# Performance work log

Measured on AMD Instinct MI355X. Metric: run time of the kernel, lower is better.

## Reference

```python
import jax, jax.numpy as jnp
import numpy as np

GRID_W, GRID_H = 4, 4          # num_splits = (4, 4) -> 16 experts
N = 524288                     # number of sample points
IN_DIM, HID, OUT = 2, 256, 3   # per-expert MLP: 2 -> 256 -> 3


def setup_inputs() -> dict:
    key = jax.random.key(0)
    k_s, k_w1, k_w2 = jax.random.split(key, 3)
    E = GRID_W * GRID_H
    samples = jax.random.uniform(k_s, (N, IN_DIM), dtype=jnp.float32)
    W1 = jax.random.normal(k_w1, (E, IN_DIM, HID), dtype=jnp.float32) * (1.0 / np.sqrt(IN_DIM))
    b1 = jnp.zeros((E, HID), dtype=jnp.float32)
    W2 = jax.random.normal(k_w2, (E, HID, OUT), dtype=jnp.float32) * (1.0 / np.sqrt(HID))
    b2 = jnp.zeros((E, OUT), dtype=jnp.float32)
    return {"samples": samples, "W1": W1, "b1": b1, "W2": W2, "b2": b2}


def _grid_inds(samples):
    # i, j = floor(samples[:, d] * n).clip(0, n-1); inds = j * w + i
    i = jnp.clip(jnp.floor(samples[:, 0] * GRID_W), 0, GRID_W - 1)
    j = jnp.clip(jnp.floor(samples[:, 1] * GRID_H), 0, GRID_H - 1)
    return (j * GRID_W + i).astype(jnp.int32)  # [N]


def reference(samples, W1, b1, W2, b2):
    inds = _grid_inds(samples)                     # [N] expert id per sample
    E = W1.shape[0]
    out = jnp.zeros((samples.shape[0], W2.shape[-1]), dtype=samples.dtype)
    # Dense dispatch: loop over the small fixed set of experts (16) and
    # select each sample's own expert output via the routing mask. Same
    # math as torch's features[inds == i] gather + scatter combine.
    for e in range(E):
        h = jax.nn.relu(samples @ W1[e] + b1[e])   # [N, HID]
        y = h @ W2[e] + b2[e]                      # [N, OUT]
        out = jnp.where((inds == e)[:, None], y, out)
    return out
```

## Files before the change

### kernel.cpp

```cpp
#include <hip/hip_runtime.h>

typedef _Float16 h2 __attribute__((ext_vector_type(2)));

#define GRID_W 4
#define GRID_H 4
#define NEXP   16
#define HID    256
#define TPB    1024
#define S      2
#define SAMP   (TPB * S)
#define NWAVE  (TPB / 64)
#define WPE    1536
#define GR     192
#define MAXENT 32

#define NSLOT   (SAMP + GR)
#define OFFB_Y  (NSLOT * 8)
#define OFFB_I  (OFFB_Y + SAMP * 12)
#define LDS_BYTES (OFFB_I + 4 * (16 + 17 + 17 + 3 * MAXENT + 1))

__global__ __launch_bounds__(256) void convert_kernel(
    const float* __restrict__ W1, const float* __restrict__ b1,
    const float* __restrict__ W2, _Float16* __restrict__ wsW) {
    int t = blockIdx.x * 256 + threadIdx.x;
    int e = t >> 8, k = t & 255;
    _Float16* dst = wsW + e * WPE;
    dst[k]        = (_Float16)W1[e * 512 + k];
    dst[256 + k]  = (_Float16)W1[e * 512 + 256 + k];
    dst[512 + k]  = (_Float16)b1[e * 256 + k];
    dst[768 + k]  = (_Float16)W2[e * 768 + 3 * k];
    dst[1024 + k] = (_Float16)W2[e * 768 + 3 * k + 1];
    dst[1280 + k] = (_Float16)W2[e * 768 + 3 * k + 2];
}

union H8 { float4 f; h2 p[4]; };

template<int M>
__device__ __forceinline__ void mlp_pass(const float4* __restrict__ W4,
                                         const h2* px2, const h2* py2,
                                         float (*y)[3]) {
#pragma unroll 4
    for (int b = 0; b < 32; ++b) {
        H8 wa, wb, bb, u0, u1, u2;
        wa.f = W4[b];
        wb.f = W4[32 + b];
        bb.f = W4[64 + b];
        u0.f = W4[96 + b];
        u1.f = W4[128 + b];
        u2.f = W4[160 + b];
#pragma unroll
        for (int j = 0; j < 4; ++j) {
#pragma unroll
            for (int s = 0; s < M; ++s) {
                h2 h = __builtin_elementwise_fma(px2[s], wa.p[j],
                       __builtin_elementwise_fma(py2[s], wb.p[j], bb.p[j]));
                h2 z = (h2)(_Float16)0.0f;
                h = __builtin_elementwise_max(h, z);
                y[s][0] = __builtin_amdgcn_fdot2(h, u0.p[j], y[s][0], false);
                y[s][1] = __builtin_amdgcn_fdot2(h, u1.p[j], y[s][1], false);
                y[s][2] = __builtin_amdgcn_fdot2(h, u2.p[j], y[s][2], false);
            }
        }
    }
}

__global__ __launch_bounds__(TPB) void fused_moe_kernel(
    const float2* __restrict__ samples,
    const _Float16* __restrict__ wsW,
    const float* __restrict__ b2,
    float* __restrict__ out, int N)
{
    extern __shared__ __align__(16) char smem[];
    int2*  sSlot = (int2*)smem;
    float* sY    = (float*)(smem + OFFB_Y);
    int*   sI    = (int*)(smem + OFFB_I);
    int* sHist = sI;
    int* sOff  = sI + 16;
    int* sES   = sI + 33;
    int* sEexp = sI + 50;
    int* sEbas = sI + 50 + MAXENT;
    int* sEcnt = sI + 50 + 2 * MAXENT;
    int* sC    = sI + 50 + 3 * MAXENT;

    const int tid = threadIdx.x;
    if (tid < NEXP) sHist[tid] = 0;
    __syncthreads();

    const int base0 = blockIdx.x * SAMP;
    float px[S], py[S]; int eid[S], rank[S]; bool act[S];
#pragma unroll
    for (int s = 0; s < S; ++s) {
        int gid = base0 + s * TPB + tid;
        act[s] = gid < N;
        float2 p = act[s] ? samples[gid] : make_float2(0.f, 0.f);
        px[s] = p.x; py[s] = p.y;
        int i = (int)(p.x * (float)GRID_W); i = i < 0 ? 0 : (i > GRID_W - 1 ? GRID_W - 1 : i);
        int j = (int)(p.y * (float)GRID_H); j = j < 0 ? 0 : (j > GRID_H - 1 ? GRID_H - 1 : j);
        eid[s] = j * GRID_W + i;
        rank[s] = act[s] ? atomicAdd(&sHist[eid[s]], 1) : 0;
    }
    __syncthreads();

    if (tid == 0) {
        int acc = 0, ec = 0;
        for (int e = 0; e < NEXP; ++e) {
            sOff[e] = acc; acc += sHist[e];
            sES[e] = ec;  ec  += (sHist[e] + GR - 1) / GR;
        }
        sOff[NEXP] = acc; sES[NEXP] = ec; *sC = ec;
    }
    __syncthreads();

#pragma unroll
    for (int s = 0; s < S; ++s) {
        if (act[s]) {
            union { h2 h; int i; } u;
            u.h.x = (_Float16)px[s]; u.h.y = (_Float16)py[s];
            int2 v; v.x = u.i; v.y = s * TPB + tid;
            sSlot[sOff[eid[s]] + rank[s]] = v;
        }
    }
    int C = *sC;
    if (tid < C) {
        int e = 0;
        while (tid >= sES[e + 1]) ++e;
        int j = tid - sES[e];
        sEexp[tid] = e;
        sEbas[tid] = sOff[e] + j * GR;
        sEcnt[tid] = min(GR, sHist[e] - j * GR);
    }
    __syncthreads();

    const int lane = tid & 63, wv = tid >> 6;
    for (int c = wv; c < C; c += NWAVE) {
        int e   = __builtin_amdgcn_readfirstlane(sEexp[c]);
        int bas = __builtin_amdgcn_readfirstlane(sEbas[c]);
        int cnt = __builtin_amdgcn_readfirstlane(sEcnt[c]);
        const float4* W4 = (const float4*)(wsW + e * WPE);
        float b20 = b2[3 * e], b21 = b2[3 * e + 1], b22 = b2[3 * e + 2];
        int m = (cnt + 63) >> 6;

        h2 px2[3], py2[3]; int ql[3]; float yy[3][3];
#pragma unroll
        for (int s = 0; s < 3; ++s) {
            if (s < m) {
                int2 v = sSlot[bas + s * 64 + lane];
                union { int i; h2 h; } u; u.i = v.x;
                px2[s].x = u.h.x; px2[s].y = u.h.x;
                py2[s].x = u.h.y; py2[s].y = u.h.y;
                ql[s] = v.y;
                yy[s][0] = b20; yy[s][1] = b21; yy[s][2] = b22;
            }
        }

        if (m == 3)      mlp_pass<3>(W4, px2, py2, yy);
        else if (m == 2) mlp_pass<2>(W4, px2, py2, yy);
        else             mlp_pass<1>(W4, px2, py2, yy);

#pragma unroll
        for (int s = 0; s < 3; ++s) {
            if (s < m && s * 64 + lane < cnt) {
                int d = 3 * ql[s];
                sY[d + 0] = yy[s][0];
                sY[d + 1] = yy[s][1];
                sY[d + 2] = yy[s][2];
            }
        }
    }
    __syncthreads();

    int nv = N - base0; if (nv > SAMP) nv = SAMP;
    int dmax = 3 * nv;
    float* outw = out + (size_t)base0 * 3;
#pragma unroll
    for (int r = 0; r < 3 * S; ++r) {
        int d = r * TPB + tid;
        if (d < dmax) outw[d] = sY[d];
    }
}

extern "C" void kernel_launch(void* const* d_in, const int* in_sizes, int n_in,
                              void* d_out, int out_size, void* d_ws, size_t ws_size,
                              hipStream_t stream) {
    const float* samples = (const float*)d_in[0];
    const float* W1      = (const float*)d_in[1];
    const float* b1      = (const float*)d_in[2];
    const float* W2      = (const float*)d_in[3];
    const float* b2      = (const float*)d_in[4];
    float* out = (float*)d_out;

    const int N = in_sizes[0] / 2;
    _Float16* wsW = (_Float16*)d_ws;

    convert_kernel<<<NEXP, 256, 0, stream>>>(W1, b1, W2, wsW);

    const int nblocks = (N + SAMP - 1) / SAMP;
    fused_moe_kernel<<<nblocks, TPB, LDS_BYTES, stream>>>(
        (const float2*)samples, wsW, b2, out, N);
}
```

Baseline: 86.50 us.

## Fold always-active hidden units into per-expert affine map, skip dead units

A prep kernel uses interval bounds over each expert's grid cell to sort hidden units into three groups: always active, which are folded into a 2->3 fp32 affine map; never active, which are dropped; and mixed, which are packed into a compact fp16 list. The main kernel evaluates the affine part in fp32 and loops only over the mixed units. Group size drops from 192 to 64 samples, and slots now carry fp32 coordinates in 16-byte entries. This cuts per-sample work in proportion to the fraction of units whose ReLU is constant inside the cell, at the cost of more chunks per block and extra LDS for slots.

```diff
diff --git a/kernel.cpp b/kernel.cpp
--- a/kernel.cpp
+++ b/kernel.cpp
@@ -10,68 +10,94 @@
 #define S      2
 #define SAMP   (TPB * S)
 #define NWAVE  (TPB / 64)
-#define WPE    1536
-#define GR     192
-#define MAXENT 32
+#define GR     64
+#define MAXENT 48
 
 #define NSLOT   (SAMP + GR)
-#define OFFB_Y  (NSLOT * 8)
+#define OFFB_Y  (NSLOT * 16)
 #define OFFB_I  (OFFB_Y + SAMP * 12)
 #define LDS_BYTES (OFFB_I + 4 * (16 + 17 + 17 + 3 * MAXENT + 1))
 
-__global__ __launch_bounds__(256) void convert_kernel(
+#define WPE_H2  768
+#define WSOFF_M2  768
+#define WSOFF_MIX 4096
+
+union H8 { float4 f; h2 p[4]; };
+
+__global__ __launch_bounds__(256) void prep_kernel(
     const float* __restrict__ W1, const float* __restrict__ b1,
-    const float* __restrict__ W2, _Float16* __restrict__ wsW) {
-    int t = blockIdx.x * 256 + threadIdx.x;
-    int e = t >> 8, k = t & 255;
-    _Float16* dst = wsW + e * WPE;
-    dst[k]        = (_Float16)W1[e * 512 + k];
-    dst[256 + k]  = (_Float16)W1[e * 512 + 256 + k];
-    dst[512 + k]  = (_Float16)b1[e * 256 + k];
-    dst[768 + k]  = (_Float16)W2[e * 768 + 3 * k];
-    dst[1024 + k] = (_Float16)W2[e * 768 + 3 * k + 1];
-    dst[1280 + k] = (_Float16)W2[e * 768 + 3 * k + 2];
-}
-
-union H8 { float4 f; h2 p[4]; };
-
-template<int M>
-__device__ __forceinline__ void mlp_pass(const float4* __restrict__ W4,
-                                         const h2* px2, const h2* py2,
-                                         float (*y)[3]) {
-#pragma unroll 4
-    for (int b = 0; b < 32; ++b) {
-        H8 wa, wb, bb, u0, u1, u2;
-        wa.f = W4[b];
-        wb.f = W4[32 + b];
-        bb.f = W4[64 + b];
-        u0.f = W4[96 + b];
-        u1.f = W4[128 + b];
-        u2.f = W4[160 + b];
-#pragma unroll
-        for (int j = 0; j < 4; ++j) {
-#pragma unroll
-            for (int s = 0; s < M; ++s) {
-                h2 h = __builtin_elementwise_fma(px2[s], wa.p[j],
-                       __builtin_elementwise_fma(py2[s], wb.p[j], bb.p[j]));
-                h2 z = (h2)(_Float16)0.0f;
-                h = __builtin_elementwise_max(h, z);
-                y[s][0] = __builtin_amdgcn_fdot2(h, u0.p[j], y[s][0], false);
-                y[s][1] = __builtin_amdgcn_fdot2(h, u1.p[j], y[s][1], false);
-                y[s][2] = __builtin_amdgcn_fdot2(h, u2.p[j], y[s][2], false);
-            }
-        }
+    const float* __restrict__ W2, const float* __restrict__ b2,
+    float* __restrict__ wsAff, int* __restrict__ wsM2,
+    _Float16* __restrict__ wsMix) {
+    __shared__ float sA[9];
+    __shared__ int sCnt;
+    __shared__ _Float16 tA[256], tB[256], tC[256], tU0[256], tU1[256], tU2[256];
+
+    const int e = blockIdx.x, k = threadIdx.x;
+    if (k < 9) sA[k] = 0.f;
+    if (k == 0) sCnt = 0;
+    __syncthreads();
+
+    float a  = W1[e * 512 + k];
+    float b  = W1[e * 512 + 256 + k];
+    float c  = b1[e * 256 + k];
+    float u0 = W2[e * 768 + 3 * k];
+    float u1 = W2[e * 768 + 3 * k + 1];
+    float u2 = W2[e * 768 + 3 * k + 2];
+
+    int ci = e & 3, cj = e >> 2;
+    float x0 = ci * 0.25f, x1 = x0 + 0.25f;
+    float y0 = cj * 0.25f, y1 = y0 + 0.25f;
+    float vmin = fminf(a * x0, a * x1) + fminf(b * y0, b * y1) + c;
+    float vmax = fmaxf(a * x0, a * x1) + fmaxf(b * y0, b * y1) + c;
+
+    if (vmin >= 0.f) {
+        atomicAdd(&sA[0], u0 * a); atomicAdd(&sA[1], u0 * b); atomicAdd(&sA[2], u0 * c);
+        atomicAdd(&sA[3], u1 * a); atomicAdd(&sA[4], u1 * b); atomicAdd(&sA[5], u1 * c);
+        atomicAdd(&sA[6], u2 * a); atomicAdd(&sA[7], u2 * b); atomicAdd(&sA[8], u2 * c);
+    } else if (vmax > 0.f) {
+        int p = atomicAdd(&sCnt, 1);
+        tA[p] = (_Float16)a;  tB[p] = (_Float16)b;  tC[p] = (_Float16)c;
+        tU0[p] = (_Float16)u0; tU1[p] = (_Float16)u1; tU2[p] = (_Float16)u2;
+    }
+    __syncthreads();
+
+    int M = sCnt;
+    int M2r = (((M + 1) >> 1) + 3) & ~3;
+    for (int t = M + k; t < 2 * M2r; t += 256) {
+        tA[t] = (_Float16)0.f; tB[t] = (_Float16)0.f; tC[t] = (_Float16)0.f;
+        tU0[t] = (_Float16)0.f; tU1[t] = (_Float16)0.f; tU2[t] = (_Float16)0.f;
+    }
+    __syncthreads();
+
+    h2* dst = (h2*)(wsMix + (size_t)e * (2 * WPE_H2));
+    if (k < M2r) {
+        h2 v;
+        v.x = tA[2 * k];  v.y = tA[2 * k + 1];  dst[k]       = v;
+        v.x = tB[2 * k];  v.y = tB[2 * k + 1];  dst[128 + k] = v;
+        v.x = tC[2 * k];  v.y = tC[2 * k + 1];  dst[256 + k] = v;
+        v.x = tU0[2 * k]; v.y = tU0[2 * k + 1]; dst[384 + k] = v;
+        v.x = tU1[2 * k]; v.y = tU1[2 * k + 1]; dst[512 + k] = v;
+        v.x = tU2[2 * k]; v.y = tU2[2 * k + 1]; dst[640 + k] = v;
+    }
+    if (k == 0) {
+        wsM2[e] = M2r;
+        float* af = wsAff + e * 12;
+        af[0] = sA[0]; af[1] = sA[1]; af[2] = b2[3 * e]     + sA[2];
+        af[3] = sA[3]; af[4] = sA[4]; af[5] = b2[3 * e + 1] + sA[5];
+        af[6] = sA[6]; af[7] = sA[7]; af[8] = b2[3 * e + 2] + sA[8];
+        af[9] = 0.f; af[10] = 0.f; af[11] = 0.f;
     }
 }
 
 __global__ __launch_bounds__(TPB) void fused_moe_kernel(
     const float2* __restrict__ samples,
-    const _Float16* __restrict__ wsW,
-    const float* __restrict__ b2,
+    const float* __restrict__ wsAff, const int* __restrict__ wsM2,
+    const _Float16* __restrict__ wsMix,
     float* __restrict__ out, int N)
 {
     extern __shared__ __align__(16) char smem[];
-    int2*  sSlot = (int2*)smem;
+    int4*  sSlot = (int4*)smem;
     float* sY    = (float*)(smem + OFFB_Y);
     int*   sI    = (int*)(smem + OFFB_I);
     int* sHist = sI;
@@ -114,9 +140,9 @@
 #pragma unroll
     for (int s = 0; s < S; ++s) {
         if (act[s]) {
-            union { h2 h; int i; } u;
-            u.h.x = (_Float16)px[s]; u.h.y = (_Float16)py[s];
-            int2 v; v.x = u.i; v.y = s * TPB + tid;
+            int4 v;
+            v.x = __float_as_int(px[s]); v.y = __float_as_int(py[s]);
+            v.z = s * TPB + tid; v.w = 0;
             sSlot[sOff[eid[s]] + rank[s]] = v;
         }
     }
@@ -136,35 +162,46 @@
         int e   = __builtin_amdgcn_readfirstlane(sEexp[c]);
         int bas = __builtin_amdgcn_readfirstlane(sEbas[c]);
         int cnt = __builtin_amdgcn_readfirstlane(sEcnt[c]);
-        const float4* W4 = (const float4*)(wsW + e * WPE);
-        float b20 = b2[3 * e], b21 = b2[3 * e + 1], b22 = b2[3 * e + 2];
-        int m = (cnt + 63) >> 6;
-
-        h2 px2[3], py2[3]; int ql[3]; float yy[3][3];
-#pragma unroll
-        for (int s = 0; s < 3; ++s) {
-            if (s < m) {
-                int2 v = sSlot[bas + s * 64 + lane];
-                union { int i; h2 h; } u; u.i = v.x;
-                px2[s].x = u.h.x; px2[s].y = u.h.x;
-                py2[s].x = u.h.y; py2[s].y = u.h.y;
-                ql[s] = v.y;
-                yy[s][0] = b20; yy[s][1] = b21; yy[s][2] = b22;
+
+        int4 v = sSlot[bas + lane];
+        float x = __int_as_float(v.x), y = __int_as_float(v.y);
+        int ql = v.z;
+
+        const float* af = wsAff + e * 12;
+        float y0 = fmaf(x, af[0], fmaf(y, af[1], af[2]));
+        float y1 = fmaf(x, af[3], fmaf(y, af[4], af[5]));
+        float y2 = fmaf(x, af[6], fmaf(y, af[7], af[8]));
+
+        h2 px2; px2.x = (_Float16)x; px2.y = px2.x;
+        h2 py2; py2.x = (_Float16)y; py2.y = py2.x;
+
+        int nb = __builtin_amdgcn_readfirstlane(wsM2[e]) >> 2;
+        const float4* Wm = (const float4*)(wsMix + (size_t)e * (2 * WPE_H2));
+        for (int bi = 0; bi < nb; ++bi) {
+            H8 A, B, Cc, U0, U1, U2;
+            A.f  = Wm[bi];        B.f  = Wm[32 + bi];  Cc.f = Wm[64 + bi];
+            U0.f = Wm[96 + bi];   U1.f = Wm[128 + bi]; U2.f = Wm[160 + bi];
+#pragma unroll
+            for (int j = 0; j < 4; ++j) {
+                h2 h = __builtin_elementwise_fma(px2, A.p[j],
+                       __builtin_elementwise_fma(py2, B.p[j], Cc.p[j]));
+                h2 z = (h2)(_Float16)0.0f;
+                h = __builtin_elementwise_max(h, z);
+#if __has_builtin(__builtin_amdgcn_fdot2)
+                y0 = __builtin_amdgcn_fdot2(h, U0.p[j], y0, false);
+                y1 = __builtin_amdgcn_fdot2(h, U1.p[j], y1, false);
+                y2 = __builtin_amdgcn_fdot2(h, U2.p[j], y2, false);
+#else
+                y0 += (float)h.x * (float)U0.p[j].x + (float)h.y * (float)U0.p[j].y;
+                y1 += (float)h.x * (float)U1.p[j].x + (float)h.y * (float)U1.p[j].y;
+                y2 += (float)h.x * (float)U2.p[j].x + (float)h.y * (float)U2.p[j].y;
+#endif
             }
         }
 
-        if (m == 3)      mlp_pass<3>(W4, px2, py2, yy);
-        else if (m == 2) mlp_pass<2>(W4, px2, py2, yy);
-        else             mlp_pass<1>(W4, px2, py2, yy);
-
-#pragma unroll
-        for (int s = 0; s < 3; ++s) {
-            if (s < m && s * 64 + lane < cnt) {
-                int d = 3 * ql[s];
-                sY[d + 0] = yy[s][0];
-                sY[d + 1] = yy[s][1];
-                sY[d + 2] = yy[s][2];
-            }
+        if (lane < cnt) {
+            int d = 3 * ql;
+            sY[d + 0] = y0; sY[d + 1] = y1; sY[d + 2] = y2;
         }
     }
     __syncthreads();
@@ -190,11 +227,13 @@
     float* out = (float*)d_out;
 
     const int N = in_sizes[0] / 2;
-    _Float16* wsW = (_Float16*)d_ws;
-
-    convert_kernel<<<NEXP, 256, 0, stream>>>(W1, b1, W2, wsW);
+    float*    wsAff = (float*)d_ws;
+    int*      wsM2  = (int*)((char*)d_ws + WSOFF_M2);
+    _Float16* wsMix = (_Float16*)((char*)d_ws + WSOFF_MIX);
+
+    prep_kernel<<<NEXP, 256, 0, stream>>>(W1, b1, W2, b2, wsAff, wsM2, wsMix);
 
     const int nblocks = (N + SAMP - 1) / SAMP;
     fused_moe_kernel<<<nblocks, TPB, LDS_BYTES, stream>>>(
-        (const float2*)samples, wsW, b2, out, N);
+        (const float2*)samples, wsAff, wsM2, wsMix, out, N);
 }
```

Measured after the change: 84.36 us. 1.03x faster.
